# Kernel tuning notes

Measured on AMD Instinct MI355X. Metric: run time of the kernel, lower is better.

The kernel has to match this reference:

```python
import jax, jax.numpy as jnp
import numpy as np

N, NFEAT, NHID, NCLASS, NHEADS = 50000, 512, 256, 64, 8
C1 = NHID // NHEADS  # 32 per-head channels, layer 1
NEG_SLOPE = 0.2


def setup_inputs() -> dict:
    key = jax.random.key(0)
    ks = jax.random.split(key, 10)
    x = jax.random.normal(ks[0], (N, NFEAT), dtype=jnp.float32)
    edge_idx = jax.random.randint(ks[1], (2, 800000), 0, N, dtype=jnp.int64)
    s = 0.05
    return {
        "x": x,
        "edge_idx": edge_idx,
        "W1": jax.random.normal(ks[2], (NFEAT, NHEADS, C1), dtype=jnp.float32) * s,
        "a1_src": jax.random.normal(ks[3], (NHEADS, C1), dtype=jnp.float32) * s,
        "a1_dst": jax.random.normal(ks[4], (NHEADS, C1), dtype=jnp.float32) * s,
        "b1": jnp.zeros((NHID,), dtype=jnp.float32),
        "W2": jax.random.normal(ks[5], (NHID, NHEADS, NCLASS), dtype=jnp.float32) * s,
        "a2_src": jax.random.normal(ks[6], (NHEADS, NCLASS), dtype=jnp.float32) * s,
        "a2_dst": jax.random.normal(ks[7], (NHEADS, NCLASS), dtype=jnp.float32) * s,
        "b2": jnp.zeros((NCLASS,), dtype=jnp.float32),
    }


def gat_conv(x, src, dst, W, a_src, a_dst, b, concat):
    # x: [N, F_in]; W: [F_in, H, C]; a_*: [H, C]; src/dst: [E]
    h = jnp.einsum("nf,fhc->nhc", x, W)             # [N, H, C]
    e_src = jnp.sum(h * a_src, axis=-1)              # [N, H]
    e_dst = jnp.sum(h * a_dst, axis=-1)              # [N, H]
    alpha = e_src[src] + e_dst[dst]                  # [E, H]
    alpha = jnp.where(alpha > 0, alpha, NEG_SLOPE * alpha)  # leaky_relu(0.2)
    # segment softmax over incoming edges of each destination node
    m = jax.ops.segment_max(alpha, dst, num_segments=N)     # [N, H]
    m = jnp.where(jnp.isfinite(m), m, 0.0)
    e = jnp.exp(alpha - m[dst])                      # [E, H]
    z = jax.ops.segment_sum(e, dst, num_segments=N)  # [N, H]
    coef = e / z[dst]                                # [E, H]
    msg = h[src] * coef[:, :, None]                  # [E, H, C]
    out = jax.ops.segment_sum(msg, dst, num_segments=N)  # [N, H, C]
    if concat:
        out = out.reshape(N, -1)
    else:
        out = out.mean(axis=1)
    return out + b


def reference(x, edge_idx, W1, a1_src, a1_dst, b1, W2, a2_src, a2_dst, b2):
    # add self loops (PyG GATConv default)
    loop = jnp.arange(N, dtype=edge_idx.dtype)
    src = jnp.concatenate([edge_idx[0], loop])
    dst = jnp.concatenate([edge_idx[1], loop])
    h = gat_conv(x, src, dst, W1, a1_src, a1_dst, b1, concat=True)   # [N, NHID]
    h = jax.nn.relu(h)
    # dropout inactive (eval mode)
    out = gat_conv(h, src, dst, W2, a2_src, a2_dst, b2, concat=False)  # [N, NCLASS]
    return jax.nn.log_softmax(out, axis=1)
```

## Files before the change

kernel.cpp:

```cpp
#include <hip/hip_runtime.h>
#include <math.h>

#define NN 50000
#define NF 512
#define NHID 256
#define NCLASS 64
#define NHEADS 8

typedef __attribute__((ext_vector_type(8))) short bf16x8;
typedef __attribute__((ext_vector_type(4))) float f32x4;
typedef __attribute__((ext_vector_type(2))) float f32x2;
typedef __attribute__((ext_vector_type(4))) unsigned int u32x4;
typedef __attribute__((ext_vector_type(2))) unsigned int u32x2;

static __device__ __forceinline__ unsigned short f2bf(float f) {
  unsigned int u = __float_as_uint(f);
  unsigned int r = (u + 0x7fffu + ((u >> 16) & 1u)) >> 16;
  return (unsigned short)r;
}
static __device__ __forceinline__ float bf2f(unsigned short u) {
  return __uint_as_float(((unsigned int)u) << 16);
}
static __device__ __forceinline__ float2 bfpair(unsigned int u) {
  return make_float2(__uint_as_float(u << 16), __uint_as_float(u & 0xffff0000u));
}

static __device__ __forceinline__ u32x2 gld64(const void* p) {
  u32x2 r;
  asm volatile("global_load_dwordx2 %0, %1, off"
               : "=v"(r) : "v"((unsigned long long)p));
  return r;
}
static __device__ __forceinline__ int gld32i(const void* p) {
  int r;
  asm volatile("global_load_dword %0, %1, off"
               : "=v"(r) : "v"((unsigned long long)p));
  return r;
}
static __device__ __forceinline__ float gld32f(const void* p) {
  float r;
  asm volatile("global_load_dword %0, %1, off"
               : "=v"(r) : "v"((unsigned long long)p));
  return r;
}
#define VMCNT0()                                        \
  do {                                                  \
    asm volatile("s_waitcnt vmcnt(0)" ::: "memory");    \
    __builtin_amdgcn_sched_barrier(0);                  \
  } while (0)

__global__ void k_init_deg(int* deg) {
  int i = blockIdx.x * blockDim.x + threadIdx.x;
  if (i < NN) deg[i] = 1;
}

__global__ void k_count(const int* __restrict__ dst, int E0, int* deg) {
  int i = blockIdx.x * blockDim.x + threadIdx.x;
  if (i < E0) atomicAdd(&deg[dst[i]], 1);
}

__global__ __launch_bounds__(1024) void k_scan(const int* __restrict__ deg, int* offs,
                                               int* cursor) {
  __shared__ int wbase[16];
  __shared__ int srun;
  int tid = threadIdx.x;
  int lane = tid & 63;
  int wv = tid >> 6;
  if (tid == 0) srun = 0;
  __syncthreads();
  for (int base = 0; base < NN; base += 4096) {
    int i = base + tid * 4;
    int4 v;
    if (i + 3 < NN) {
      v = *(const int4*)(deg + i);
    } else {
      v.x = (i + 0 < NN) ? deg[i + 0] : 0;
      v.y = (i + 1 < NN) ? deg[i + 1] : 0;
      v.z = (i + 2 < NN) ? deg[i + 2] : 0;
      v.w = (i + 3 < NN) ? deg[i + 3] : 0;
    }
    int tot = v.x + v.y + v.z + v.w;
    int s = tot;
    #pragma unroll
    for (int o = 1; o < 64; o <<= 1) {
      int t = __shfl_up(s, o);
      if (lane >= o) s += t;
    }
    if (lane == 63) wbase[wv] = s;
    __syncthreads();
    if (tid == 0) {
      int run = srun;
      #pragma unroll
      for (int w2 = 0; w2 < 16; w2++) {
        int t = wbase[w2];
        wbase[w2] = run;
        run += t;
      }
      srun = run;
    }
    __syncthreads();
    int p = wbase[wv] + s - tot;
    if (i + 0 < NN) { offs[i + 0] = p; cursor[i + 0] = p; p += v.x; }
    if (i + 1 < NN) { offs[i + 1] = p; cursor[i + 1] = p; p += v.y; }
    if (i + 2 < NN) { offs[i + 2] = p; cursor[i + 2] = p; p += v.z; }
    if (i + 3 < NN) { offs[i + 3] = p; cursor[i + 3] = p; }
  }
  __syncthreads();
  if (tid == 0) offs[NN] = srun;
}

__global__ void k_scatter(const int* __restrict__ src, const int* __restrict__ dst,
                          int E0, int* cursor, int* __restrict__ nbr) {
  int i = blockIdx.x * blockDim.x + threadIdx.x;
  if (i < E0) {
    int pos = atomicAdd(&cursor[dst[i]], 1);
    nbr[pos] = src[i];
  } else if (i < E0 + NN) {
    int v = i - E0;
    int pos = atomicAdd(&cursor[v], 1);
    nbr[pos] = v;
  }
}

__global__ void k_cast4(const float* __restrict__ in, unsigned short* __restrict__ out,
                        int n4) {
  int i = blockIdx.x * blockDim.x + threadIdx.x;
  if (i >= n4) return;
  float4 v = *(const float4*)(in + (size_t)i * 4);
  ushort4 o;
  o.x = f2bf(v.x); o.y = f2bf(v.y); o.z = f2bf(v.z); o.w = f2bf(v.w);
  *(ushort4*)(out + (size_t)i * 4) = o;
}

__global__ void k_castWt(const float* __restrict__ W, unsigned short* __restrict__ Wt,
                         int K, int cols) {
  int i = blockIdx.x * blockDim.x + threadIdx.x;
  if (i >= K * cols) return;
  int k = i / cols, c = i % cols;
  Wt[(size_t)c * K + k] = f2bf(W[i]);
}

__global__ void k_castWt_perm(const float* __restrict__ W, unsigned short* __restrict__ Wt,
                              int K) {
  int i = blockIdx.x * blockDim.x + threadIdx.x;
  if (i >= K * NHEADS * NCLASS) return;
  int k = i / (NHEADS * NCLASS);
  int rem = i % (NHEADS * NCLASS);
  int h = rem / NCLASS, c = rem % NCLASS;
  Wt[(size_t)(c * NHEADS + h) * K + k] = f2bf(W[i]);
}

__global__ void k_cast_fp8(const unsigned short* __restrict__ in,
                           unsigned char* __restrict__ out, int n8) {
  int i = blockIdx.x * blockDim.x + threadIdx.x;
  if (i >= n8) return;
  uint4 raw = *(const uint4*)(in + (size_t)i * 8);
  float2 p0 = bfpair(raw.x), p1 = bfpair(raw.y), p2 = bfpair(raw.z), p3 = bfpair(raw.w);
  int lo = 0, hi = 0;
  lo = __builtin_amdgcn_cvt_pk_fp8_f32(p0.x, p0.y, lo, false);
  lo = __builtin_amdgcn_cvt_pk_fp8_f32(p1.x, p1.y, lo, true);
  hi = __builtin_amdgcn_cvt_pk_fp8_f32(p2.x, p2.y, hi, false);
  hi = __builtin_amdgcn_cvt_pk_fp8_f32(p3.x, p3.y, hi, true);
  u32x2 o; o[0] = (unsigned int)lo; o[1] = (unsigned int)hi;
  *(u32x2*)(out + (size_t)i * 8) = o;
}

__global__ __launch_bounds__(256) void k_gemm_bf(const unsigned short* __restrict__ A,
                                                 const unsigned short* __restrict__ Bt,
                                                 unsigned short* __restrict__ C,
                                                 int rows, int K, int cols) {
  __shared__ unsigned short Bs[256 * 40];
  int t = threadIdx.x;
  int wave = t >> 6, lane = t & 63;
  int quad = lane >> 4, sixt = lane & 15;
  int rb = blockIdx.x * 64 + (wave >> 1) * 32;
  int cw = (wave & 1) * 128;
  int cbw = blockIdx.y * 256 + cw;
  int r0 = rb + sixt, r1 = rb + 16 + sixt;
  const unsigned short* Ap0 = A + (size_t)(r0 < rows ? r0 : 0) * K + quad * 8;
  const unsigned short* Ap1 = A + (size_t)(r1 < rows ? r1 : 0) * K + quad * 8;
  const unsigned short* Bg = Bt + (size_t)(blockIdx.y * 256 + (t >> 2)) * K + (t & 3) * 8;
  const size_t BgStep = (size_t)64 * K;
  char* BsW = (char*)Bs + (t >> 2) * 80 + (t & 3) * 16;
  f32x4 acc0[8] = {}, acc1[8] = {};
  for (int k0 = 0; k0 < K; k0 += 32) {
    uint4 v0 = *(const uint4*)(Bg + k0);
    uint4 v1 = *(const uint4*)(Bg + BgStep + k0);
    uint4 v2 = *(const uint4*)(Bg + 2 * BgStep + k0);
    uint4 v3 = *(const uint4*)(Bg + 3 * BgStep + k0);
    bf16x8 a0 = *(const bf16x8*)(Ap0 + k0);
    bf16x8 a1 = *(const bf16x8*)(Ap1 + k0);
    *(uint4*)(BsW) = v0;
    *(uint4*)(BsW + 64 * 80) = v1;
    *(uint4*)(BsW + 128 * 80) = v2;
    *(uint4*)(BsW + 192 * 80) = v3;
    __syncthreads();
    #pragma unroll
    for (int g = 0; g < 8; g++) {
      bf16x8 b = *(const bf16x8*)((const char*)Bs + (cw + g * 16 + sixt) * 80 + quad * 16);
      acc0[g] = __builtin_amdgcn_mfma_f32_16x16x32_bf16(a0, b, acc0[g], 0, 0, 0);
      acc1[g] = __builtin_amdgcn_mfma_f32_16x16x32_bf16(a1, b, acc1[g], 0, 0, 0);
    }
    __syncthreads();
  }
  #pragma unroll
  for (int r = 0; r < 4; r++) {
    int row = rb + quad * 4 + r;
    if (row < rows) {
      unsigned short* out = C + (size_t)row * cols + cbw + sixt;
      #pragma unroll
      for (int g = 0; g < 8; g++) out[g * 16] = f2bf(acc0[g][r]);
    }
    int row2 = row + 16;
    if (row2 < rows) {
      unsigned short* out = C + (size_t)row2 * cols + cbw + sixt;
      #pragma unroll
      for (int g = 0; g < 8; g++) out[g * 16] = f2bf(acc1[g][r]);
    }
  }
}

__global__ __launch_bounds__(256) void k_gemm_bf8(const unsigned short* __restrict__ A,
                                                  const unsigned short* __restrict__ Bt,
                                                  unsigned char* __restrict__ C,
                                                  int rows, int K, int cols) {
  __shared__ unsigned short Bs[256 * 40];
  int t = threadIdx.x;
  int wave = t >> 6, lane = t & 63;
  int quad = lane >> 4, sixt = lane & 15;
  int rb = blockIdx.x * 64 + (wave >> 1) * 32;
  int cw = (wave & 1) * 128;
  int cbw = blockIdx.y * 256 + cw;
  int r0 = rb + sixt, r1 = rb + 16 + sixt;
  const unsigned short* Ap0 = A + (size_t)(r0 < rows ? r0 : 0) * K + quad * 8;
  const unsigned short* Ap1 = A + (size_t)(r1 < rows ? r1 : 0) * K + quad * 8;
  const unsigned short* Bg = Bt + (size_t)(blockIdx.y * 256 + (t >> 2)) * K + (t & 3) * 8;
  const size_t BgStep = (size_t)64 * K;
  char* BsW = (char*)Bs + (t >> 2) * 80 + (t & 3) * 16;
  f32x4 acc0[8] = {}, acc1[8] = {};
  for (int k0 = 0; k0 < K; k0 += 32) {
    uint4 v0 = *(const uint4*)(Bg + k0);
    uint4 v1 = *(const uint4*)(Bg + BgStep + k0);
    uint4 v2 = *(const uint4*)(Bg + 2 * BgStep + k0);
    uint4 v3 = *(const uint4*)(Bg + 3 * BgStep + k0);
    bf16x8 a0 = *(const bf16x8*)(Ap0 + k0);
    bf16x8 a1 = *(const bf16x8*)(Ap1 + k0);
    *(uint4*)(BsW) = v0;
    *(uint4*)(BsW + 64 * 80) = v1;
    *(uint4*)(BsW + 128 * 80) = v2;
    *(uint4*)(BsW + 192 * 80) = v3;
    __syncthreads();
    #pragma unroll
    for (int g = 0; g < 8; g++) {
      bf16x8 b = *(const bf16x8*)((const char*)Bs + (cw + g * 16 + sixt) * 80 + quad * 16);
      acc0[g] = __builtin_amdgcn_mfma_f32_16x16x32_bf16(a0, b, acc0[g], 0, 0, 0);
      acc1[g] = __builtin_amdgcn_mfma_f32_16x16x32_bf16(a1, b, acc1[g], 0, 0, 0);
    }
    __syncthreads();
  }
  #pragma unroll
  for (int r = 0; r < 4; r++) {
    int row = rb + quad * 4 + r;
    if (row < rows) {
      unsigned char* out = C + (size_t)row * cols + cbw + sixt;
      #pragma unroll
      for (int g = 0; g < 8; g++) {
        int wq = __builtin_amdgcn_cvt_pk_fp8_f32(acc0[g][r], acc0[g][r], 0, false);
        out[g * 16] = (unsigned char)(wq & 0xff);
      }
    }
    int row2 = row + 16;
    if (row2 < rows) {
      unsigned char* out = C + (size_t)row2 * cols + cbw + sixt;
      #pragma unroll
      for (int g = 0; g < 8; g++) {
        int wq = __builtin_amdgcn_cvt_pk_fp8_f32(acc1[g][r], acc1[g][r], 0, false);
        out[g * 16] = (unsigned char)(wq & 0xff);
      }
    }
  }
}

template <int C>
__global__ void k_escore_c(const unsigned short* __restrict__ h,
                           const float* __restrict__ asr, const float* __restrict__ ads,
                           float* __restrict__ es, float* __restrict__ ed) {
  int idx = blockIdx.x * blockDim.x + threadIdx.x;
  if (idx >= NN * NHEADS) return;
  int hd = idx & 7;
  const unsigned short* row = h + (size_t)idx * C;
  float s = 0.f, d = 0.f;
  #pragma unroll
  for (int c8 = 0; c8 < C / 8; c8++) {
    uint4 raw = *(const uint4*)(row + c8 * 8);
    float2 p0 = bfpair(raw.x), p1 = bfpair(raw.y), p2 = bfpair(raw.z), p3 = bfpair(raw.w);
    const float* as_ = asr + hd * C + c8 * 8;
    const float* ad_ = ads + hd * C + c8 * 8;
    s += p0.x * as_[0] + p0.y * as_[1] + p1.x * as_[2] + p1.y * as_[3] +
         p2.x * as_[4] + p2.y * as_[5] + p3.x * as_[6] + p3.y * as_[7];
    d += p0.x * ad_[0] + p0.y * ad_[1] + p1.x * ad_[2] + p1.y * ad_[3] +
         p2.x * ad_[4] + p2.y * ad_[5] + p3.x * ad_[6] + p3.y * ad_[7];
  }
  es[idx] = s;
  ed[idx] = d;
}

__global__ void k_escore_p8(const unsigned char* __restrict__ h,
                            const float* __restrict__ asr, const float* __restrict__ ads,
                            float* __restrict__ es, float* __restrict__ ed) {
  int idx = blockIdx.x * blockDim.x + threadIdx.x;
  if (idx >= NN * NHEADS) return;
  int hd = idx & 7;
  int n = idx >> 3;
  const unsigned short* rp =
      (const unsigned short*)(h + (size_t)n * (NHEADS * NCLASS) + (hd & ~1));
  int hi = hd & 1;
  float s = 0.f, d = 0.f;
  #pragma unroll
  for (int c = 0; c < NCLASS; c++) {
    unsigned short w = rp[c * 4];
    f32x2 q = __builtin_amdgcn_cvt_pk_f32_fp8((int)w, false);
    float v = hi ? q.y : q.x;
    s += v * asr[hd * NCLASS + c];
    d += v * ads[hd * NCLASS + c];
  }
  es[idx] = s;
  ed[idx] = d;
}

__global__ __launch_bounds__(256) void k_agg1f(const int* __restrict__ offs,
                                               const int* __restrict__ nbr,
                                               const unsigned char* __restrict__ h1f8,
                                               const float* __restrict__ es,
                                               const float* __restrict__ ed,
                                               const float* __restrict__ b1,
                                               unsigned short* __restrict__ out) {
  int node = blockIdx.x * 4 + (threadIdx.x >> 6);
  if (node >= NN) return;
  int lane = threadIdx.x & 63;
  int h = lane & 7;
  int sub = lane >> 3;
  int col = lane << 2;
  int beg = offs[node], end = offs[node + 1];
  float edst = ed[node * NHEADS + h];
  int kb = beg;
  int iA = kb + (lane & 7); if (iA > end - 1) iA = end - 1;
  int vt = gld32i(nbr + iA);
  int vtN = 0;
  if (kb + 8 < end) {
    int iB = kb + 8 + (lane & 7); if (iB > end - 1) iB = end - 1;
    vtN = gld32i(nbr + iB);
  }
  VMCNT0();
  int se[8];
  #pragma unroll
  for (int e = 0; e < 8; e++) se[e] = __shfl(vt, e);
  float esv;
  {
    int sv = __shfl(vt, sub);
    esv = gld32f(es + (size_t)sv * NHEADS + h);
  }
  VMCNT0();
  float m = -1e30f, z = 0.f;
  float4 acc = make_float4(0.f, 0.f, 0.f, 0.f);
  while (true) {
    int cnt = end - kb; if (cnt > 8) cnt = 8;
    int r[8];
    #pragma unroll
    for (int e = 0; e < 8; e++)
      if (e < cnt) r[e] = gld32i(h1f8 + (size_t)se[e] * NHID + col);
    bool more = kb + 8 < end, more2 = kb + 16 < end;
    int vt2 = 0;
    if (more2) {
      int iC = kb + 16 + (lane & 7); if (iC > end - 1) iC = end - 1;
      vt2 = gld32i(nbr + iC);
    }
    float esvN = 0.f;
    if (more) {
      int svN = __shfl(vtN, sub);
      esvN = gld32f(es + (size_t)svN * NHEADS + h);
    }
    float ar = esv + edst;
    ar = (ar > 0.f) ? ar : 0.2f * ar;
    float a = (kb + sub < end) ? ar : -1e30f;
    float gm = a;
    #pragma unroll
    for (int o = 8; o < 64; o <<= 1) gm = fmaxf(gm, __shfl_xor(gm, o));
    float mn = fmaxf(m, gm);
    float ee = __expf(a - mn);
    float zg = ee;
    #pragma unroll
    for (int o = 8; o < 64; o <<= 1) zg += __shfl_xor(zg, o);
    float sc = __expf(m - mn);
    z = z * sc + zg;
    m = mn;
    VMCNT0();
    float sch = __shfl(sc, sub);
    acc.x *= sch; acc.y *= sch; acc.z *= sch; acc.w *= sch;
    #pragma unroll
    for (int e = 0; e < 8; e++) {
      if (e < cnt) {
        float ce = __shfl(ee, e * 8 + sub);
        f32x2 q0 = __builtin_amdgcn_cvt_pk_f32_fp8(r[e], false);
        f32x2 q1 = __builtin_amdgcn_cvt_pk_f32_fp8(r[e], true);
        acc.x += ce * q0.x;
        acc.y += ce * q0.y;
        acc.z += ce * q1.x;
        acc.w += ce * q1.y;
      }
    }
    if (!more) break;
    kb += 8;
    #pragma unroll
    for (int e = 0; e < 8; e++) se[e] = __shfl(vtN, e);
    esv = esvN;
    vtN = vt2;
  }
  float inv = 1.f / z;
  float ivh = __shfl(inv, sub);
  ushort4 o;
  o.x = f2bf(fmaxf(acc.x * ivh + b1[col + 0], 0.f));
  o.y = f2bf(fmaxf(acc.y * ivh + b1[col + 1], 0.f));
  o.z = f2bf(fmaxf(acc.z * ivh + b1[col + 2], 0.f));
  o.w = f2bf(fmaxf(acc.w * ivh + b1[col + 3], 0.f));
  *(ushort4*)(out + (size_t)node * NHID + col) = o;
}

__global__ __launch_bounds__(256) void k_agg2f(const int* __restrict__ offs,
                                               const int* __restrict__ nbr,
                                               const unsigned char* __restrict__ h2f8,
                                               const float* __restrict__ es,
                                               const float* __restrict__ ed,
                                               const float* __restrict__ b2,
                                               float* __restrict__ out) {
  __shared__ __align__(16) float cs[4][64];
  int wv = threadIdx.x >> 6;
  int node = blockIdx.x * 4 + wv;
  if (node >= NN) return;
  int lane = threadIdx.x & 63;
  int h = lane & 7;
  int sub = lane >> 3;
  int beg = offs[node], end = offs[node + 1];
  float edst = ed[node * NHEADS + h];
  int kb = beg;
  int iA = kb + (lane & 7); if (iA > end - 1) iA = end - 1;
  int vt = gld32i(nbr + iA);
  int vtN = 0;
  if (kb + 8 < end) {
    int iB = kb + 8 + (lane & 7); if (iB > end - 1) iB = end - 1;
    vtN = gld32i(nbr + iB);
  }
  VMCNT0();
  int se[8];
  #pragma unroll
  for (int e = 0; e < 8; e++) se[e] = __shfl(vt, e);
  float esv;
  {
    int sv = __shfl(vt, sub);
    esv = gld32f(es + (size_t)sv * NHEADS + h);
  }
  VMCNT0();
  float m = -1e30f, z = 0.f;
  float acc[8] = {};
  while (true) {
    int cnt = end - kb; if (cnt > 8) cnt = 8;
    u32x2 r[8];
    #pragma unroll
    for (int e = 0; e < 8; e++)
      if (e < cnt) r[e] = gld64(h2f8 + (size_t)se[e] * (NHEADS * NCLASS) + (lane << 3));
    bool more = kb + 8 < end, more2 = kb + 16 < end;
    int vt2 = 0;
    if (more2) {
      int iC = kb + 16 + (lane & 7); if (iC > end - 1) iC = end - 1;
      vt2 = gld32i(nbr + iC);
    }
    float esvN = 0.f;
    if (more) {
      int svN = __shfl(vtN, sub);
      esvN = gld32f(es + (size_t)svN * NHEADS + h);
    }
    float ar = esv + edst;
    ar = (ar > 0.f) ? ar : 0.2f * ar;
    float a = (kb + sub < end) ? ar : -1e30f;
    float gm = a;
    #pragma unroll
    for (int o = 8; o < 64; o <<= 1) gm = fmaxf(gm, __shfl_xor(gm, o));
    float mn = fmaxf(m, gm);
    float ee = __expf(a - mn);
    float zg = ee;
    #pragma unroll
    for (int o = 8; o < 64; o <<= 1) zg += __shfl_xor(zg, o);
    float sc = __expf(m - mn);
    z = z * sc + zg;
    m = mn;
    cs[wv][lane] = ee;
    VMCNT0();
    #pragma unroll
    for (int hh = 0; hh < 8; hh++) acc[hh] *= __shfl(sc, hh);
    #pragma unroll
    for (int e = 0; e < 8; e++) {
      if (e < cnt) {
        float4 cA = *(const float4*)&cs[wv][e * 8];
        float4 cB = *(const float4*)&cs[wv][e * 8 + 4];
        f32x2 q0 = __builtin_amdgcn_cvt_pk_f32_fp8((int)r[e][0], false);
        f32x2 q1 = __builtin_amdgcn_cvt_pk_f32_fp8((int)r[e][0], true);
        f32x2 q2 = __builtin_amdgcn_cvt_pk_f32_fp8((int)r[e][1], false);
        f32x2 q3 = __builtin_amdgcn_cvt_pk_f32_fp8((int)r[e][1], true);
        acc[0] += cA.x * q0.x;
        acc[1] += cA.y * q0.y;
        acc[2] += cA.z * q1.x;
        acc[3] += cA.w * q1.y;
        acc[4] += cB.x * q2.x;
        acc[5] += cB.y * q2.y;
        acc[6] += cB.z * q3.x;
        acc[7] += cB.w * q3.y;
      }
    }
    if (!more) break;
    kb += 8;
    #pragma unroll
    for (int e = 0; e < 8; e++) se[e] = __shfl(vtN, e);
    esv = esvN;
    vtN = vt2;
  }
  float inv = 1.f / z;
  float val = 0.f;
  #pragma unroll
  for (int hh = 0; hh < 8; hh++) val += acc[hh] * __shfl(inv, hh);
  val = val * 0.125f + b2[lane];
  float mx = val;
  #pragma unroll
  for (int o = 32; o > 0; o >>= 1) mx = fmaxf(mx, __shfl_xor(mx, o));
  float ex = __expf(val - mx);
  float sm = ex;
  #pragma unroll
  for (int o = 32; o > 0; o >>= 1) sm += __shfl_xor(sm, o);
  out[(size_t)node * NCLASS + lane] = val - mx - __logf(sm);
}

extern "C" void kernel_launch(void* const* d_in, const int* in_sizes, int n_in,
                              void* d_out, int out_size, void* d_ws, size_t ws_size,
                              hipStream_t stream) {
  const float* x   = (const float*)d_in[0];
  const int* eidx  = (const int*)d_in[1];
  const float* W1  = (const float*)d_in[2];
  const float* a1s = (const float*)d_in[3];
  const float* a1d = (const float*)d_in[4];
  const float* b1  = (const float*)d_in[5];
  const float* W2  = (const float*)d_in[6];
  const float* a2s = (const float*)d_in[7];
  const float* a2d = (const float*)d_in[8];
  const float* b2  = (const float*)d_in[9];
  const int E0 = in_sizes[1] / 2;
  const int* esrc = eidx;
  const int* edst = eidx + E0;
  const int E = E0 + NN;

  char* w = (char*)d_ws;
  auto carve = [&](size_t bytes) {
    void* p = (void*)w;
    w += (bytes + 255) & ~(size_t)255;
    return p;
  };
  int* deg      = (int*)carve((size_t)NN * 4);
  int* offs     = (int*)carve((size_t)(NN + 1) * 4);
  int* cursor   = (int*)carve((size_t)NN * 4);
  int* nbr      = (int*)carve((size_t)E * 4);
  float* es1    = (float*)carve((size_t)NN * NHEADS * 4);
  float* ed1    = (float*)carve((size_t)NN * NHEADS * 4);
  unsigned short* xbf   = (unsigned short*)carve((size_t)NN * NF * 2);
  unsigned short* W1t   = (unsigned short*)carve((size_t)NF * NHID * 2);
  unsigned short* W2t   = (unsigned short*)carve((size_t)NHID * NHEADS * NCLASS * 2);
  unsigned short* h1b   = (unsigned short*)carve((size_t)NN * NHID * 2);
  unsigned short* out1b = (unsigned short*)carve((size_t)NN * NHID * 2);
  unsigned char* h1f8   = (unsigned char*)carve((size_t)NN * NHID);
  unsigned char* h2f8 = (unsigned char*)xbf;

  k_init_deg<<<(NN + 255) / 256, 256, 0, stream>>>(deg);
  k_count<<<(E0 + 255) / 256, 256, 0, stream>>>(edst, E0, deg);
  k_scan<<<1, 1024, 0, stream>>>(deg, offs, cursor);
  k_scatter<<<(E0 + NN + 255) / 256, 256, 0, stream>>>(esrc, edst, E0, cursor, nbr);

  k_cast4<<<(NN * NF / 4 + 255) / 256, 256, 0, stream>>>(x, xbf, NN * NF / 4);
  k_castWt<<<(NF * NHID + 255) / 256, 256, 0, stream>>>(W1, W1t, NF, NHID);
  k_castWt_perm<<<(NHID * NHEADS * NCLASS + 255) / 256, 256, 0, stream>>>(W2, W2t, NHID);

  k_gemm_bf<<<dim3((NN + 63) / 64, NHID / 256), 256, 0, stream>>>(xbf, W1t, h1b,
                                                                  NN, NF, NHID);
  k_escore_c<32><<<(NN * NHEADS + 255) / 256, 256, 0, stream>>>(h1b, a1s, a1d, es1, ed1);
  k_cast_fp8<<<(NN * NHID / 8 + 255) / 256, 256, 0, stream>>>(h1b, h1f8, NN * NHID / 8);
  k_agg1f<<<(NN + 3) / 4, 256, 0, stream>>>(offs, nbr, h1f8, es1, ed1, b1, out1b);

  k_gemm_bf8<<<dim3((NN + 63) / 64, (NHEADS * NCLASS) / 256), 256, 0, stream>>>(
      out1b, W2t, h2f8, NN, NHID, NHEADS * NCLASS);
  k_escore_p8<<<(NN * NHEADS + 255) / 256, 256, 0, stream>>>(h2f8, a2s, a2d, es1, ed1);
  k_agg2f<<<(NN + 3) / 4, 256, 0, stream>>>(offs, nbr, h2f8, es1, ed1, b2,
                                            (float*)d_out);
}
```

Measured before the change: 548.0 us.

## Fuse input casts into first GEMM, emit fp8 copy, parallelize CSR scan

The first GEMM now reads fp32 x directly and converts it to bf16 in registers, which removes the separate x-to-bf16 cast pass and its intermediate buffer. Its epilogue also writes an fp8 copy of h1 alongside the bf16 output, so the standalone bf16-to-fp8 cast kernel is gone. The single-block serial scan is replaced by a three-kernel multi-block scan (block-local scans, a scan of block sums, then an add-back pass). In exchange the GEMM reads twice as many bytes of A per tile and does byte-wide fp8 stores, and the scan now costs three kernel launches instead of one.

```diff
diff --git a/kernel.cpp b/kernel.cpp
--- a/kernel.cpp
+++ b/kernel.cpp
@@ -6,11 +6,11 @@
 #define NHID 256
 #define NCLASS 64
 #define NHEADS 8
+#define SCAN_NBLK ((NN + 1023) / 1024)
 
 typedef __attribute__((ext_vector_type(8))) short bf16x8;
 typedef __attribute__((ext_vector_type(4))) float f32x4;
 typedef __attribute__((ext_vector_type(2))) float f32x2;
-typedef __attribute__((ext_vector_type(4))) unsigned int u32x4;
 typedef __attribute__((ext_vector_type(2))) unsigned int u32x2;
 
 static __device__ __forceinline__ unsigned short f2bf(float f) {
@@ -23,6 +23,17 @@
 }
 static __device__ __forceinline__ float2 bfpair(unsigned int u) {
   return make_float2(__uint_as_float(u << 16), __uint_as_float(u & 0xffff0000u));
+}
+
+static __device__ __forceinline__ bf16x8 cvt8(float4 lo, float4 hi) {
+  unsigned int w0, w1, w2, w3;
+  asm("v_cvt_pk_bf16_f32 %0, %1, %2" : "=v"(w0) : "v"(lo.x), "v"(lo.y));
+  asm("v_cvt_pk_bf16_f32 %0, %1, %2" : "=v"(w1) : "v"(lo.z), "v"(lo.w));
+  asm("v_cvt_pk_bf16_f32 %0, %1, %2" : "=v"(w2) : "v"(hi.x), "v"(hi.y));
+  asm("v_cvt_pk_bf16_f32 %0, %1, %2" : "=v"(w3) : "v"(hi.z), "v"(hi.w));
+  union { unsigned int u[4]; bf16x8 b; } p;
+  p.u[0] = w0; p.u[1] = w1; p.u[2] = w2; p.u[3] = w3;
+  return p.b;
 }
 
 static __device__ __forceinline__ u32x2 gld64(const void* p) {
@@ -59,54 +70,68 @@
   if (i < E0) atomicAdd(&deg[dst[i]], 1);
 }
 
-__global__ __launch_bounds__(1024) void k_scan(const int* __restrict__ deg, int* offs,
-                                               int* cursor) {
-  __shared__ int wbase[16];
-  __shared__ int srun;
+__global__ __launch_bounds__(256) void k_scanA(const int* __restrict__ deg, int* offs,
+                                               int* bsum) {
+  __shared__ int wsum[4];
   int tid = threadIdx.x;
   int lane = tid & 63;
   int wv = tid >> 6;
-  if (tid == 0) srun = 0;
+  int i = blockIdx.x * 1024 + tid * 4;
+  int4 v = make_int4(0, 0, 0, 0);
+  if (i + 3 < NN) {
+    v = *(const int4*)(deg + i);
+  } else {
+    if (i + 0 < NN) v.x = deg[i + 0];
+    if (i + 1 < NN) v.y = deg[i + 1];
+    if (i + 2 < NN) v.z = deg[i + 2];
+    if (i + 3 < NN) v.w = deg[i + 3];
+  }
+  int tot = v.x + v.y + v.z + v.w;
+  int s = tot;
+  #pragma unroll
+  for (int o = 1; o < 64; o <<= 1) {
+    int t = __shfl_up(s, o);
+    if (lane >= o) s += t;
+  }
+  if (lane == 63) wsum[wv] = s;
   __syncthreads();
-  for (int base = 0; base < NN; base += 4096) {
-    int i = base + tid * 4;
-    int4 v;
-    if (i + 3 < NN) {
-      v = *(const int4*)(deg + i);
-    } else {
-      v.x = (i + 0 < NN) ? deg[i + 0] : 0;
-      v.y = (i + 1 < NN) ? deg[i + 1] : 0;
-      v.z = (i + 2 < NN) ? deg[i + 2] : 0;
-      v.w = (i + 3 < NN) ? deg[i + 3] : 0;
-    }
-    int tot = v.x + v.y + v.z + v.w;
-    int s = tot;
-    #pragma unroll
-    for (int o = 1; o < 64; o <<= 1) {
-      int t = __shfl_up(s, o);
-      if (lane >= o) s += t;
-    }
-    if (lane == 63) wbase[wv] = s;
-    __syncthreads();
-    if (tid == 0) {
-      int run = srun;
-      #pragma unroll
-      for (int w2 = 0; w2 < 16; w2++) {
-        int t = wbase[w2];
-        wbase[w2] = run;
-        run += t;
-      }
-      srun = run;
-    }
-    __syncthreads();
-    int p = wbase[wv] + s - tot;
-    if (i + 0 < NN) { offs[i + 0] = p; cursor[i + 0] = p; p += v.x; }
-    if (i + 1 < NN) { offs[i + 1] = p; cursor[i + 1] = p; p += v.y; }
-    if (i + 2 < NN) { offs[i + 2] = p; cursor[i + 2] = p; p += v.z; }
-    if (i + 3 < NN) { offs[i + 3] = p; cursor[i + 3] = p; }
-  }
-  __syncthreads();
-  if (tid == 0) offs[NN] = srun;
+  int base = 0;
+  #pragma unroll
+  for (int w2 = 0; w2 < 4; w2++)
+    if (w2 < wv) base += wsum[w2];
+  int p = base + s - tot;
+  if (i + 0 < NN) { offs[i + 0] = p; p += v.x; }
+  if (i + 1 < NN) { offs[i + 1] = p; p += v.y; }
+  if (i + 2 < NN) { offs[i + 2] = p; p += v.z; }
+  if (i + 3 < NN) { offs[i + 3] = p; }
+  if (tid == 255) bsum[blockIdx.x] = base + s;
+}
+
+__global__ void k_scanB(const int* __restrict__ bsum, int* bbase, int* offs, int nb) {
+  int lane = threadIdx.x;
+  int v = (lane < nb) ? bsum[lane] : 0;
+  int s = v;
+  #pragma unroll
+  for (int o = 1; o < 64; o <<= 1) {
+    int t = __shfl_up(s, o);
+    if (lane >= o) s += t;
+  }
+  if (lane < nb) bbase[lane] = s - v;
+  if (lane == 63) offs[NN] = s;
+}
+
+__global__ __launch_bounds__(256) void k_scanC(int* offs, int* cursor,
+                                               const int* __restrict__ bbase) {
+  int add = bbase[blockIdx.x];
+  int i = blockIdx.x * 1024 + threadIdx.x * 4;
+  #pragma unroll
+  for (int j = 0; j < 4; j++) {
+    if (i + j < NN) {
+      int o = offs[i + j] + add;
+      offs[i + j] = o;
+      cursor[i + j] = o;
+    }
+  }
 }
 
 __global__ void k_scatter(const int* __restrict__ src, const int* __restrict__ dst,
@@ -122,16 +147,6 @@
   }
 }
 
-__global__ void k_cast4(const float* __restrict__ in, unsigned short* __restrict__ out,
-                        int n4) {
-  int i = blockIdx.x * blockDim.x + threadIdx.x;
-  if (i >= n4) return;
-  float4 v = *(const float4*)(in + (size_t)i * 4);
-  ushort4 o;
-  o.x = f2bf(v.x); o.y = f2bf(v.y); o.z = f2bf(v.z); o.w = f2bf(v.w);
-  *(ushort4*)(out + (size_t)i * 4) = o;
-}
-
 __global__ void k_castWt(const float* __restrict__ W, unsigned short* __restrict__ Wt,
                          int K, int cols) {
   int i = blockIdx.x * blockDim.x + threadIdx.x;
@@ -150,25 +165,10 @@
   Wt[(size_t)(c * NHEADS + h) * K + k] = f2bf(W[i]);
 }
 
-__global__ void k_cast_fp8(const unsigned short* __restrict__ in,
-                           unsigned char* __restrict__ out, int n8) {
-  int i = blockIdx.x * blockDim.x + threadIdx.x;
-  if (i >= n8) return;
-  uint4 raw = *(const uint4*)(in + (size_t)i * 8);
-  float2 p0 = bfpair(raw.x), p1 = bfpair(raw.y), p2 = bfpair(raw.z), p3 = bfpair(raw.w);
-  int lo = 0, hi = 0;
-  lo = __builtin_amdgcn_cvt_pk_fp8_f32(p0.x, p0.y, lo, false);
-  lo = __builtin_amdgcn_cvt_pk_fp8_f32(p1.x, p1.y, lo, true);
-  hi = __builtin_amdgcn_cvt_pk_fp8_f32(p2.x, p2.y, hi, false);
-  hi = __builtin_amdgcn_cvt_pk_fp8_f32(p3.x, p3.y, hi, true);
-  u32x2 o; o[0] = (unsigned int)lo; o[1] = (unsigned int)hi;
-  *(u32x2*)(out + (size_t)i * 8) = o;
-}
-
-__global__ __launch_bounds__(256) void k_gemm_bf(const unsigned short* __restrict__ A,
-                                                 const unsigned short* __restrict__ Bt,
-                                                 unsigned short* __restrict__ C,
-                                                 int rows, int K, int cols) {
+__global__ __launch_bounds__(256) void k_gemm_f32a_dual(
+    const float* __restrict__ A, const unsigned short* __restrict__ Bt,
+    unsigned short* __restrict__ C, unsigned char* __restrict__ C8,
+    int rows, int K, int cols) {
   __shared__ unsigned short Bs[256 * 40];
   int t = threadIdx.x;
   int wave = t >> 6, lane = t & 63;
@@ -177,8 +177,8 @@
   int cw = (wave & 1) * 128;
   int cbw = blockIdx.y * 256 + cw;
   int r0 = rb + sixt, r1 = rb + 16 + sixt;
-  const unsigned short* Ap0 = A + (size_t)(r0 < rows ? r0 : 0) * K + quad * 8;
-  const unsigned short* Ap1 = A + (size_t)(r1 < rows ? r1 : 0) * K + quad * 8;
+  const float* Ap0 = A + (size_t)(r0 < rows ? r0 : 0) * K + quad * 8;
+  const float* Ap1 = A + (size_t)(r1 < rows ? r1 : 0) * K + quad * 8;
   const unsigned short* Bg = Bt + (size_t)(blockIdx.y * 256 + (t >> 2)) * K + (t & 3) * 8;
   const size_t BgStep = (size_t)64 * K;
   char* BsW = (char*)Bs + (t >> 2) * 80 + (t & 3) * 16;
@@ -188,8 +188,12 @@
     uint4 v1 = *(const uint4*)(Bg + BgStep + k0);
     uint4 v2 = *(const uint4*)(Bg + 2 * BgStep + k0);
     uint4 v3 = *(const uint4*)(Bg + 3 * BgStep + k0);
-    bf16x8 a0 = *(const bf16x8*)(Ap0 + k0);
-    bf16x8 a1 = *(const bf16x8*)(Ap1 + k0);
+    float4 a0lo = *(const float4*)(Ap0 + k0);
+    float4 a0hi = *(const float4*)(Ap0 + k0 + 4);
+    float4 a1lo = *(const float4*)(Ap1 + k0);
+    float4 a1hi = *(const float4*)(Ap1 + k0 + 4);
+    bf16x8 a0 = cvt8(a0lo, a0hi);
+    bf16x8 a1 = cvt8(a1lo, a1hi);
     *(uint4*)(BsW) = v0;
     *(uint4*)(BsW + 64 * 80) = v1;
     *(uint4*)(BsW + 128 * 80) = v2;
@@ -208,14 +212,24 @@
     int row = rb + quad * 4 + r;
     if (row < rows) {
       unsigned short* out = C + (size_t)row * cols + cbw + sixt;
+      unsigned char* out8 = C8 + (size_t)row * cols + cbw + sixt;
       #pragma unroll
-      for (int g = 0; g < 8; g++) out[g * 16] = f2bf(acc0[g][r]);
+      for (int g = 0; g < 8; g++) {
+        out[g * 16] = f2bf(acc0[g][r]);
+        int wq = __builtin_amdgcn_cvt_pk_fp8_f32(acc0[g][r], acc0[g][r], 0, false);
+        out8[g * 16] = (unsigned char)(wq & 0xff);
+      }
     }
     int row2 = row + 16;
     if (row2 < rows) {
       unsigned short* out = C + (size_t)row2 * cols + cbw + sixt;
+      unsigned char* out8 = C8 + (size_t)row2 * cols + cbw + sixt;
       #pragma unroll
-      for (int g = 0; g < 8; g++) out[g * 16] = f2bf(acc1[g][r]);
+      for (int g = 0; g < 8; g++) {
+        out[g * 16] = f2bf(acc1[g][r]);
+        int wq = __builtin_amdgcn_cvt_pk_fp8_f32(acc1[g][r], acc1[g][r], 0, false);
+        out8[g * 16] = (unsigned char)(wq & 0xff);
+      }
     }
   }
 }
@@ -566,29 +580,30 @@
   int* offs     = (int*)carve((size_t)(NN + 1) * 4);
   int* cursor   = (int*)carve((size_t)NN * 4);
   int* nbr      = (int*)carve((size_t)E * 4);
+  int* bsum     = (int*)carve((size_t)64 * 4);
+  int* bbase    = (int*)carve((size_t)64 * 4);
   float* es1    = (float*)carve((size_t)NN * NHEADS * 4);
   float* ed1    = (float*)carve((size_t)NN * NHEADS * 4);
-  unsigned short* xbf   = (unsigned short*)carve((size_t)NN * NF * 2);
   unsigned short* W1t   = (unsigned short*)carve((size_t)NF * NHID * 2);
   unsigned short* W2t   = (unsigned short*)carve((size_t)NHID * NHEADS * NCLASS * 2);
   unsigned short* h1b   = (unsigned short*)carve((size_t)NN * NHID * 2);
   unsigned short* out1b = (unsigned short*)carve((size_t)NN * NHID * 2);
   unsigned char* h1f8   = (unsigned char*)carve((size_t)NN * NHID);
-  unsigned char* h2f8 = (unsigned char*)xbf;
+  unsigned char* h2f8   = (unsigned char*)carve((size_t)NN * NHEADS * NCLASS);
 
   k_init_deg<<<(NN + 255) / 256, 256, 0, stream>>>(deg);
   k_count<<<(E0 + 255) / 256, 256, 0, stream>>>(edst, E0, deg);
-  k_scan<<<1, 1024, 0, stream>>>(deg, offs, cursor);
+  k_scanA<<<SCAN_NBLK, 256, 0, stream>>>(deg, offs, bsum);
+  k_scanB<<<1, 64, 0, stream>>>(bsum, bbase, offs, SCAN_NBLK);
+  k_scanC<<<SCAN_NBLK, 256, 0, stream>>>(offs, cursor, bbase);
   k_scatter<<<(E0 + NN + 255) / 256, 256, 0, stream>>>(esrc, edst, E0, cursor, nbr);
 
-  k_cast4<<<(NN * NF / 4 + 255) / 256, 256, 0, stream>>>(x, xbf, NN * NF / 4);
   k_castWt<<<(NF * NHID + 255) / 256, 256, 0, stream>>>(W1, W1t, NF, NHID);
   k_castWt_perm<<<(NHID * NHEADS * NCLASS + 255) / 256, 256, 0, stream>>>(W2, W2t, NHID);
 
-  k_gemm_bf<<<dim3((NN + 63) / 64, NHID / 256), 256, 0, stream>>>(xbf, W1t, h1b,
-                                                                  NN, NF, NHID);
+  k_gemm_f32a_dual<<<dim3((NN + 63) / 64, NHID / 256), 256, 0, stream>>>(
+      x, W1t, h1b, h1f8, NN, NF, NHID);
   k_escore_c<32><<<(NN * NHEADS + 255) / 256, 256, 0, stream>>>(h1b, a1s, a1d, es1, ed1);
-  k_cast_fp8<<<(NN * NHID / 8 + 255) / 256, 256, 0, stream>>>(h1b, h1f8, NN * NHID / 8);
   k_agg1f<<<(NN + 3) / 4, 256, 0, stream>>>(offs, nbr, h1f8, es1, ed1, b1, out1b);
 
   k_gemm_bf8<<<dim3((NN + 63) / 64, (NHEADS * NCLASS) / 256), 256, 0, stream>>>(
```

Result: faster. 523.1 us (-4.5%).
